# Kernel tuning notes

Measured on AMD Instinct MI355X. Metric: run time of the kernel, lower is better.

The kernel has to match this reference:

```python
import jax, jax.numpy as jnp
import numpy as np

# Static config (matches init_kwargs)
B, H, W, C = 16, 56, 56, 512
WS, SHIFT, NH = 7, 3, 16
HD = C // NH
N = WS * WS
NW = (H // WS) * (W // WS)
SCALE = HD ** -0.5
EPS = 1e-5


def _relative_position_index():
    coords = np.stack(np.meshgrid(np.arange(WS), np.arange(WS), indexing='ij'))  # (2,WS,WS)
    flat = coords.reshape(2, -1)                       # (2,N)
    rel = flat[:, :, None] - flat[:, None, :]          # (2,N,N)
    rel = rel.transpose(1, 2, 0).astype(np.int64)
    rel[..., 0] += WS - 1
    rel[..., 1] += WS - 1
    rel[..., 0] *= 2 * WS - 1
    return rel.sum(-1)                                 # (N,N)


def _window_partition_np(x):
    # x: (H,W) numpy -> (NW, N)
    return x.reshape(H // WS, WS, W // WS, WS).transpose(0, 2, 1, 3).reshape(-1, N)


def _attn_mask():
    img = np.zeros((H, W))
    cnt = 0
    for hs in (slice(0, -WS), slice(-WS, -SHIFT), slice(-SHIFT, None)):
        for ws_ in (slice(0, -WS), slice(-WS, -SHIFT), slice(-SHIFT, None)):
            img[hs, ws_] = cnt
            cnt += 1
    mw = _window_partition_np(img)                     # (NW, N)
    diff = mw[:, None, :] - mw[:, :, None]             # (NW, N, N)
    return np.where(diff != 0, -100.0, 0.0).astype(np.float32)


REL_IDX = jnp.asarray(_relative_position_index())
ATTN_MASK = jnp.asarray(_attn_mask())


def window_partition(x):
    # x: (B,H,W,C) -> (B*NW, N, C)
    x = x.reshape(B, H // WS, WS, W // WS, WS, C)
    return x.transpose(0, 1, 3, 2, 4, 5).reshape(-1, N, C)


def window_reverse(w):
    # w: (B*NW, N, C) -> (B,H,W,C)
    x = w.reshape(B, H // WS, W // WS, WS, WS, C)
    return x.transpose(0, 1, 3, 2, 4, 5).reshape(B, H, W, C)


def layer_norm(x, g, b):
    m = x.mean(-1, keepdims=True)
    v = jnp.mean((x - m) ** 2, axis=-1, keepdims=True)
    return (x - m) * jax.lax.rsqrt(v + EPS) * g + b


def before_cross_attention(x, g, b):
    # x: (B, L, C) -> shifted windows (B*NW, N, C)
    x = layer_norm(x, g, b).reshape(B, H, W, C)
    x = jnp.roll(x, (-SHIFT, -SHIFT), axis=(1, 2))
    return window_partition(x)


def get_qkv(x, Wqkv, bqkv):
    # x: (B_, N, C); Wqkv: (C, 3C)
    qkv = (x @ Wqkv + bqkv).reshape(-1, N, 3, NH, HD).transpose(2, 0, 3, 1, 4)
    return qkv[0], qkv[1], qkv[2]  # each (B_, NH, N, HD)


def setup_inputs() -> dict:
    key = jax.random.key(0)
    ks = jax.random.split(key, 10)
    s = 0.02
    return {
        'rescaled': jax.random.normal(ks[0], (B, H * W, C), jnp.float32),
        'rescaler': jax.random.normal(ks[1], (B, H * W, C), jnp.float32),
        'gamma_a': jnp.ones((C,), jnp.float32),
        'beta_a': jnp.zeros((C,), jnp.float32),
        'gamma_b': jnp.ones((C,), jnp.float32),
        'beta_b': jnp.zeros((C,), jnp.float32),
        'Wqkv_a': jax.random.normal(ks[2], (C, 3 * C), jnp.float32) * s,
        'bqkv_a': jnp.zeros((3 * C,), jnp.float32),
        'Wqkv_b': jax.random.normal(ks[3], (C, 3 * C), jnp.float32) * s,
        'bqkv_b': jnp.zeros((3 * C,), jnp.float32),
        'rpb_table': jax.random.normal(ks[4], ((2 * WS - 1) ** 2, NH), jnp.float32) * s,
        'Wproj': jax.random.normal(ks[5], (C, C), jnp.float32) * s,
        'bproj': jnp.zeros((C,), jnp.float32),
    }


def reference(rescaled, rescaler, gamma_a, beta_a, gamma_b, beta_b,
              Wqkv_a, bqkv_a, Wqkv_b, bqkv_b, rpb_table, Wproj, bproj):
    # norm + shift + window partition for both streams
    xw = before_cross_attention(rescaled, gamma_a, beta_a)   # (B*NW, N, C)
    yw = before_cross_attention(rescaler, gamma_b, beta_b)

    q_a, k_a, v_a = get_qkv(xw, Wqkv_a, bqkv_a)  # rescaled stream
    q_b, k_b, v_b = get_qkv(yw, Wqkv_b, bqkv_b)  # rescaler stream
    # same_key_query=False: q from rescaler, k & v from rescaled
    q, k, v = q_b * SCALE, k_a, v_a

    attn = jnp.einsum('bhnd,bhmd->bhnm', q, k)               # (B*NW, NH, N, N)
    rpb = rpb_table[REL_IDX.reshape(-1)].reshape(N, N, NH).transpose(2, 0, 1)
    attn = attn + rpb[None]
    attn = attn.reshape(B, NW, NH, N, N) + ATTN_MASK[None, :, None]
    attn = jax.nn.softmax(attn.reshape(-1, NH, N, N), axis=-1)

    out = jnp.einsum('bhnm,bhmd->bhnd', attn, v)             # (B*NW, NH, N, HD)
    out = out.transpose(0, 2, 1, 3).reshape(-1, N, C)
    out = out @ Wproj + bproj

    # window reverse + un-shift, back to (B, L, C)
    x = window_reverse(out)
    x = jnp.roll(x, (SHIFT, SHIFT), axis=(1, 2))
    return x.reshape(B, H * W, C)
```

## Files before the change

kernel.cpp:

```cpp
#include <hip/hip_runtime.h>
#include <hip/hip_bf16.h>


typedef short bf16x8 __attribute__((ext_vector_type(8)));
typedef float f32x4 __attribute__((ext_vector_type(4)));
typedef unsigned short u16;

#define MTOT 50176
#define SCALE_ 0.17677669529663687f

__device__ __forceinline__ u16 f2bf(float f) {
    __hip_bfloat16 h = __float2bfloat16(f);
    return *reinterpret_cast<u16*>(&h);
}
__device__ __forceinline__ float bf2f(u16 u) {
    union { unsigned int i; float f; } t; t.i = ((unsigned int)u) << 16; return t.f;
}

#define ASYNC_COPY16(g, l)                                                      \
    __builtin_amdgcn_global_load_lds((__attribute__((address_space(1))) void*)(g), \
                                     (__attribute__((address_space(3))) void*)(l), 16, 0, 0)

__global__ __launch_bounds__(256) void wconv_kernel(
    const float* __restrict__ Wqkv_a, const float* __restrict__ Wqkv_b,
    const float* __restrict__ Wproj, u16* __restrict__ Wt)
{
    const int idx = blockIdx.x * 256 + threadIdx.x;
    const int r = idx >> 9;
    const int k = idx & 511;
    float val;
    if (r < 512)       val = Wqkv_b[k * 1536 + r];
    else if (r < 1536) val = Wqkv_a[k * 1536 + r];
    else               val = Wproj[k * 512 + (r - 1536)];
    Wt[idx] = f2bf(val);
}

__global__ __launch_bounds__(256) void build_bias_kernel(
    const float* __restrict__ rpb, float* __restrict__ biasT)
{
    const int blk = blockIdx.x;
    const int mid = blk >> 4, head = blk & 15;
    const int whq = (mid >> 1) & 1, wwq = mid & 1;
    for (int t = threadIdx.x; t < 4096; t += 256) {
        const int col = t >> 6, row = t & 63;
        float v;
        if (row < 49 && col < 49) {
            const int ih = row / 7, iw = row - ih * 7;
            const int jh = col / 7, jw = col - jh * 7;
            v = rpb[((ih - jh + 6) * 13 + (iw - jw + 6)) * 16 + head];
            const int li = (whq ? (ih < 4 ? 1 : 2) : 0) * 3 + (wwq ? (iw < 4 ? 1 : 2) : 0);
            const int lj = (whq ? (jh < 4 ? 1 : 2) : 0) * 3 + (wwq ? (jw < 4 ? 1 : 2) : 0);
            if (li != lj) v -= 100.0f;
        } else {
            v = -3.0e38f;
        }
        biasT[(size_t)blk * 4096 + t] = v;
    }
}

__device__ __forceinline__ void ln_one(
    const float* __restrict__ src, const float* __restrict__ g,
    const float* __restrict__ bt, u16* __restrict__ dst, int lane)
{
    const float4 v0 = *(const float4*)(src + lane * 8);
    const float4 v1 = *(const float4*)(src + lane * 8 + 4);
    float s = v0.x + v0.y + v0.z + v0.w + v1.x + v1.y + v1.z + v1.w;
    float q = v0.x*v0.x + v0.y*v0.y + v0.z*v0.z + v0.w*v0.w
            + v1.x*v1.x + v1.y*v1.y + v1.z*v1.z + v1.w*v1.w;
#pragma unroll
    for (int o = 32; o >= 1; o >>= 1) { s += __shfl_xor(s, o); q += __shfl_xor(q, o); }
    const float mean = s * (1.0f / 512.0f);
    const float rstd = rsqrtf(q * (1.0f / 512.0f) - mean * mean + 1e-5f);
    const float4 g0 = *(const float4*)(g + lane * 8);
    const float4 g1 = *(const float4*)(g + lane * 8 + 4);
    const float4 b0 = *(const float4*)(bt + lane * 8);
    const float4 b1 = *(const float4*)(bt + lane * 8 + 4);
    u16 o8[8];
    o8[0] = f2bf((v0.x - mean) * rstd * g0.x + b0.x);
    o8[1] = f2bf((v0.y - mean) * rstd * g0.y + b0.y);
    o8[2] = f2bf((v0.z - mean) * rstd * g0.z + b0.z);
    o8[3] = f2bf((v0.w - mean) * rstd * g0.w + b0.w);
    o8[4] = f2bf((v1.x - mean) * rstd * g1.x + b1.x);
    o8[5] = f2bf((v1.y - mean) * rstd * g1.y + b1.y);
    o8[6] = f2bf((v1.z - mean) * rstd * g1.z + b1.z);
    o8[7] = f2bf((v1.w - mean) * rstd * g1.w + b1.w);
    int4 pk;
    pk.x = (int)(((unsigned)o8[1] << 16) | o8[0]);
    pk.y = (int)(((unsigned)o8[3] << 16) | o8[2]);
    pk.z = (int)(((unsigned)o8[5] << 16) | o8[4]);
    pk.w = (int)(((unsigned)o8[7] << 16) | o8[6]);
    *(int4*)(dst + lane * 8) = pk;
}

__global__ __launch_bounds__(256) void ln_window_kernel(
    const float* __restrict__ xa, const float* __restrict__ xb,
    const float* __restrict__ ga, const float* __restrict__ bea,
    const float* __restrict__ gb, const float* __restrict__ beb,
    u16* __restrict__ xw, u16* __restrict__ yw)
{
    const int wave = threadIdx.x >> 6, lane = threadIdx.x & 63;
    const int row = blockIdx.x * 4 + wave;
    const int win = row / 49, n = row - win * 49;
    const int b = win >> 6, wi = win & 63;
    const int wh = wi >> 3, ww = wi & 7;
    const int ih = n / 7, iw = n - ih * 7;
    int h = wh * 7 + ih + 3; if (h >= 56) h -= 56;
    int w = ww * 7 + iw + 3; if (w >= 56) w -= 56;
    const size_t src = ((size_t)b * 3136 + (size_t)h * 56 + w) * 512;
    const size_t dst = (size_t)row * 512;
    ln_one(xa + src, ga, bea, xw + dst, lane);
    ln_one(xb + src, gb, beb, yw + dst, lane);
}

#define GEMM8P_MAIN()                                                           \
    __shared__ __align__(16) u16 As[2][128 * 32];                               \
    __shared__ __align__(16) u16 Bs[2][256 * 32];                               \
    const int tid = threadIdx.x;                                                \
    const int lane = tid & 63;                                                  \
    const int wv = tid >> 6;                                                    \
    const int wm = wv >> 2, wn = wv & 3;                                        \
    const int rowl = lane & 15, kg = lane >> 4;                                 \
    const int fsw = (rowl >> 1) & 3;               \
    f32x4 acc[4][4];                                                            \
    for (int i = 0; i < 4; ++i)                                                 \
        for (int j = 0; j < 4; ++j)                                             \
            acc[i][j] = (f32x4){0.f, 0.f, 0.f, 0.f};                            \
    const int srow = tid >> 2;                                      \
    const int scol = ((tid & 3) ^ ((tid >> 3) & 3)) * 8;      \
    const u16* Ab  = Asrc + (size_t)(mt * 128 + srow) * 512 + scol;             \
    const u16* Bb0 = Bsrc + (size_t)srow * 512 + scol;                          \
    const u16* Bb1 = Bsrc + (size_t)(128 + srow) * 512 + scol;                  \
                                        \
    ASYNC_COPY16(Ab,  (char*)&As[0][0] + tid * 16);                             \
    ASYNC_COPY16(Bb0, (char*)&Bs[0][0] + tid * 16);                             \
    ASYNC_COPY16(Bb1, (char*)&Bs[0][0] + 8192 + tid * 16);                      \
    asm volatile("s_waitcnt vmcnt(0)" ::: "memory");                            \
    __syncthreads();                                                            \
    for (int kt = 0; kt < 16; ++kt) {                                           \
        const int cur = kt & 1, nxt = cur ^ 1;                                  \
        if (kt < 15) {                                                          \
            const int k1 = (kt + 1) * 32;                                       \
            ASYNC_COPY16(Ab + k1,  (char*)&As[0][0] + nxt * 8192 + tid * 16);   \
            ASYNC_COPY16(Bb0 + k1, (char*)&Bs[0][0] + nxt * 16384 + tid * 16);  \
            ASYNC_COPY16(Bb1 + k1, (char*)&Bs[0][0] + nxt * 16384 + 8192 + tid * 16); \
        }                                                                       \
        const u16* Asb = &As[cur][0];                                           \
        const u16* Bsb = &Bs[cur][0];                                           \
        bf16x8 af[4], bfr[4];                                                   \
        _Pragma("unroll")                                                       \
        for (int i = 0; i < 4; ++i)                                             \
            af[i] = *(const bf16x8*)(Asb + (wm * 64 + i * 16 + rowl) * 32       \
                                         + ((kg ^ fsw) * 8));                   \
        _Pragma("unroll")                                                       \
        for (int j = 0; j < 4; ++j)                                             \
            bfr[j] = *(const bf16x8*)(Bsb + (wn * 64 + j * 16 + rowl) * 32      \
                                          + ((kg ^ fsw) * 8));                  \
        _Pragma("unroll")                                                       \
        for (int i = 0; i < 4; ++i) {                                           \
            _Pragma("unroll")                                                   \
            for (int j = 0; j < 4; ++j)                                         \
                acc[i][j] = __builtin_amdgcn_mfma_f32_16x16x32_bf16(            \
                    af[i], bfr[j], acc[i][j], 0, 0, 0);                         \
        }                                                                       \
        asm volatile("s_waitcnt vmcnt(0)" ::: "memory");                        \
        __syncthreads();                                                        \
    }

__global__ __launch_bounds__(512) void gemm_qkv_kernel(
    const u16* __restrict__ xw, const u16* __restrict__ yw,
    const u16* __restrict__ Wt,
    const float* __restrict__ bqkv_a, const float* __restrict__ bqkv_b,
    u16* __restrict__ qb, u16* __restrict__ kb, u16* __restrict__ vb)
{
    const int bid = blockIdx.x;
    const int swz = (bid & 7) * 294 + (bid >> 3);
    const int nt = swz % 6;
    const int mt = swz / 6;
    const u16* Asrc = (nt < 2) ? yw : xw;
    const u16* Bsrc = Wt + (size_t)(nt * 256) * 512;
    GEMM8P_MAIN()

    u16* dst; const float* bvec; bool isq = false;
    if (nt < 2)      { dst = qb; bvec = bqkv_b; isq = true; }
    else if (nt < 4) { dst = kb; bvec = bqkv_a; }
    else             { dst = vb; bvec = bqkv_a; }
#pragma unroll
    for (int j = 0; j < 4; ++j) {
        const int col = nt * 256 + wn * 64 + j * 16 + rowl;
        const float bias_ = bvec[col];
        const int pcol = col & 511;
#pragma unroll
        for (int i = 0; i < 4; ++i) {
#pragma unroll
            for (int rr = 0; rr < 4; ++rr) {
                const int row = mt * 128 + wm * 64 + i * 16 + kg * 4 + rr;
                float val = acc[i][j][rr] + bias_;
                if (isq) val *= SCALE_;
                dst[(size_t)row * 512 + pcol] = f2bf(val);
            }
        }
    }
}

__global__ __launch_bounds__(512) void gemm_proj_kernel(
    const u16* __restrict__ attn_out, const u16* __restrict__ WtProj,
    const float* __restrict__ bproj, float* __restrict__ out)
{
    const int bid = blockIdx.x;
    const int swz = (bid & 7) * 98 + (bid >> 3);
    const int nt = swz & 1;
    const int mt = swz >> 1;
    const u16* Asrc = attn_out;
    const u16* Bsrc = WtProj + (size_t)(nt * 256) * 512;
    GEMM8P_MAIN()

#pragma unroll
    for (int j = 0; j < 4; ++j) {
        const int col = nt * 256 + wn * 64 + j * 16 + rowl;
        const float bias_ = bproj[col];
#pragma unroll
        for (int i = 0; i < 4; ++i) {
#pragma unroll
            for (int rr = 0; rr < 4; ++rr) {
                const int row = mt * 128 + wm * 64 + i * 16 + kg * 4 + rr;
                const int win = row / 49;
                const int nw = row - win * 49;
                const int b = win >> 6, wi = win & 63;
                const int wh = wi >> 3, ww = wi & 7;
                const int ih = nw / 7, iw = nw - ih * 7;
                int h = wh * 7 + ih + 3; if (h >= 56) h -= 56;
                int w = ww * 7 + iw + 3; if (w >= 56) w -= 56;
                out[((size_t)b * 3136 + (size_t)h * 56 + w) * 512 + col] =
                    acc[i][j][rr] + bias_;
            }
        }
    }
}

__global__ __launch_bounds__(256) void attn_kernel(
    const u16* __restrict__ qb, const u16* __restrict__ kb,
    const u16* __restrict__ vb, const float* __restrict__ biasT,
    u16* __restrict__ attn_out)
{
    __shared__ __align__(16) u16 VT[32 * 64];
    __shared__ __align__(16) u16 P[64 * 64];
    const int tid = threadIdx.x;
    const int wh_id = blockIdx.x;
    const int win = wh_id >> 4, head = wh_id & 15;
    const int lane = tid & 63, wvi = tid >> 6;
    const int rowl = lane & 15, kg = lane >> 4;
    const size_t base = (size_t)win * 49 * 512 + head * 32;

    {
        const int j = tid >> 2, d0 = (tid & 3) * 8;
        const bf16x8 v8 = *(const bf16x8*)(vb + base + (size_t)j * 512 + d0);
        const int cj = j >> 3, je = j & 7;
#pragma unroll
        for (int m = 0; m < 8; ++m) {
            const int d = d0 + m;
            VT[d * 64 + ((cj ^ (d & 7)) * 8) + je] = (u16)v8[m];
        }
    }

    const bf16x8 aq = *(const bf16x8*)(qb + base + (size_t)(wvi * 16 + rowl) * 512 + kg * 8);
    f32x4 accS[4];
#pragma unroll
    for (int j = 0; j < 4; ++j) {
        const bf16x8 bk = *(const bf16x8*)(kb + base + (size_t)(j * 16 + rowl) * 512 + kg * 8);
        accS[j] = __builtin_amdgcn_mfma_f32_16x16x32_bf16(
            aq, bk, (f32x4){0.f, 0.f, 0.f, 0.f}, 0, 0, 0);
    }

    const int wi = win & 63;
    const int mid = (((wi >> 3) == 7) ? 2 : 0) + (((wi & 7) == 7) ? 1 : 0);
    const float* bptr = biasT + ((size_t)(mid * 16 + head) << 12);
#pragma unroll
    for (int j = 0; j < 4; ++j) {
        const f32x4 bv4 = *(const f32x4*)(bptr + (j * 16 + rowl) * 64 + wvi * 16 + kg * 4);
#pragma unroll
        for (int r = 0; r < 4; ++r)
            accS[j][r] += bv4[r];
    }

    float rinv[4];
#pragma unroll
    for (int r = 0; r < 4; ++r) {
        float m = fmaxf(fmaxf(accS[0][r], accS[1][r]), fmaxf(accS[2][r], accS[3][r]));
#pragma unroll
        for (int o = 1; o <= 8; o <<= 1) m = fmaxf(m, __shfl_xor(m, o));
        float s = 0.f;
#pragma unroll
        for (int j = 0; j < 4; ++j) {
            accS[j][r] = __expf(accS[j][r] - m);
            s += accS[j][r];
        }
#pragma unroll
        for (int o = 1; o <= 8; o <<= 1) s += __shfl_xor(s, o);
        rinv[r] = __frcp_rn(s);
    }

#pragma unroll
    for (int j = 0; j < 4; ++j) {
        const int c = j * 2 + (rowl >> 3);
#pragma unroll
        for (int r = 0; r < 4; ++r) {
            const int row = wvi * 16 + kg * 4 + r;
            P[row * 64 + ((c ^ (row & 7)) * 8) + (rowl & 7)] = f2bf(accS[j][r]);
        }
    }

    __syncthreads();

    f32x4 accO[2];
#pragma unroll
    for (int dt = 0; dt < 2; ++dt) {
        accO[dt] = (f32x4){0.f, 0.f, 0.f, 0.f};
#pragma unroll
        for (int kb_ = 0; kb_ < 2; ++kb_) {
            const int prow = wvi * 16 + rowl;
            const int ca = kb_ * 4 + kg;
            const bf16x8 ap = *(const bf16x8*)(P + prow * 64 + ((ca ^ (prow & 7)) * 8));
            const int vd = dt * 16 + rowl;
            const bf16x8 bv = *(const bf16x8*)(VT + vd * 64 + ((ca ^ (vd & 7)) * 8));
            accO[dt] = __builtin_amdgcn_mfma_f32_16x16x32_bf16(ap, bv, accO[dt], 0, 0, 0);
        }
    }

#pragma unroll
    for (int dt = 0; dt < 2; ++dt) {
#pragma unroll
        for (int r = 0; r < 4; ++r) {
            const int i = wvi * 16 + kg * 4 + r;
            if (i < 49)
                attn_out[base + (size_t)i * 512 + dt * 16 + rowl] =
                    f2bf(accO[dt][r] * rinv[r]);
        }
    }
}

extern "C" void kernel_launch(void* const* d_in, const int* in_sizes, int n_in,
                              void* d_out, int out_size, void* d_ws, size_t ws_size,
                              hipStream_t stream) {
    (void)in_sizes; (void)n_in; (void)out_size; (void)ws_size;
    const float* rescaled = (const float*)d_in[0];
    const float* rescaler = (const float*)d_in[1];
    const float* gamma_a  = (const float*)d_in[2];
    const float* beta_a   = (const float*)d_in[3];
    const float* gamma_b  = (const float*)d_in[4];
    const float* beta_b   = (const float*)d_in[5];
    const float* Wqkv_a   = (const float*)d_in[6];
    const float* bqkv_a   = (const float*)d_in[7];
    const float* Wqkv_b   = (const float*)d_in[8];
    const float* bqkv_b   = (const float*)d_in[9];
    const float* rpb      = (const float*)d_in[10];
    const float* Wproj    = (const float*)d_in[11];
    const float* bproj    = (const float*)d_in[12];
    float* out = (float*)d_out;

    char* ws = (char*)d_ws;
    const size_t SZ = (size_t)MTOT * 512 * 2;
    u16* xw = (u16*)ws;
    u16* yw = (u16*)(ws + SZ);
    u16* qb = (u16*)(ws + 2 * SZ);
    u16* kb = (u16*)(ws + 3 * SZ);
    u16* vb = (u16*)(ws + 4 * SZ);
    u16* Wt = (u16*)(ws + 5 * SZ);
    float* biasT = (float*)(ws + 5 * SZ + 2097152);
    u16* attn_out = xw;

    wconv_kernel<<<4096, 256, 0, stream>>>(Wqkv_a, Wqkv_b, Wproj, Wt);
    build_bias_kernel<<<64, 256, 0, stream>>>(rpb, biasT);
    ln_window_kernel<<<MTOT / 4, 256, 0, stream>>>(
        rescaled, rescaler, gamma_a, beta_a, gamma_b, beta_b, xw, yw);
    gemm_qkv_kernel<<<2352, 512, 0, stream>>>(
        xw, yw, Wt, bqkv_a, bqkv_b, qb, kb, vb);
    attn_kernel<<<16384, 256, 0, stream>>>(qb, kb, vb, biasT, attn_out);
    gemm_proj_kernel<<<784, 512, 0, stream>>>(
        attn_out, Wt + (size_t)1536 * 512, bproj, out);
}
```

Measured before the change: 534.4 us.

## Overlap GEMM tile loads with MFMA and tile weight transpose through LDS

The shared GEMM main loop now issues the next K-tile's async global-to-LDS copies, waits only for the previous batch with vmcnt(3), and then computes. The last tile is peeled out, so each iteration's loads overlap with its MFMA work instead of being drained with vmcnt(0) after the math. Separately, the weight conversion kernel transposes 64x64 tiles through padded shared memory, using coalesced float4 reads and 16-byte bf16 writes instead of strided scalar reads. This adds an extra barrier per iteration and relies on the vmcnt accounting being correct for the double buffer.

```diff
diff --git a/kernel.cpp b/kernel.cpp
--- a/kernel.cpp
+++ b/kernel.cpp
@@ -25,14 +25,43 @@
     const float* __restrict__ Wqkv_a, const float* __restrict__ Wqkv_b,
     const float* __restrict__ Wproj, u16* __restrict__ Wt)
 {
-    const int idx = blockIdx.x * 256 + threadIdx.x;
-    const int r = idx >> 9;
-    const int k = idx & 511;
-    float val;
-    if (r < 512)       val = Wqkv_b[k * 1536 + r];
-    else if (r < 1536) val = Wqkv_a[k * 1536 + r];
-    else               val = Wproj[k * 512 + (r - 1536)];
-    Wt[idx] = f2bf(val);
+    __shared__ float tile[64][65];
+    const int rt = blockIdx.x >> 3;
+    const int kt = blockIdx.x & 7;
+    const int r0 = rt * 64, k0 = kt * 64;
+    const float* src; int stride, c0;
+    if (r0 < 512)       { src = Wqkv_b; stride = 1536; c0 = r0; }
+    else if (r0 < 1536) { src = Wqkv_a; stride = 1536; c0 = r0; }
+    else                { src = Wproj;  stride = 512;  c0 = r0 - 1536; }
+
+    const int tid = threadIdx.x;
+    const int sr = tid >> 4, sc = (tid & 15) * 4;
+#pragma unroll
+    for (int p = 0; p < 4; ++p) {
+        const int k = sr + p * 16;
+        const float4 v = *(const float4*)(src + (size_t)(k0 + k) * stride + c0 + sc);
+        tile[k][sc] = v.x; tile[k][sc + 1] = v.y;
+        tile[k][sc + 2] = v.z; tile[k][sc + 3] = v.w;
+    }
+    __syncthreads();
+
+    const int dc = tid >> 2;
+    const int kk = (tid & 3) * 16;
+    u16 o[16];
+#pragma unroll
+    for (int m = 0; m < 16; ++m) o[m] = f2bf(tile[kk + m][dc]);
+    int4 pk0, pk1;
+    pk0.x = (int)(((unsigned)o[1] << 16) | o[0]);
+    pk0.y = (int)(((unsigned)o[3] << 16) | o[2]);
+    pk0.z = (int)(((unsigned)o[5] << 16) | o[4]);
+    pk0.w = (int)(((unsigned)o[7] << 16) | o[6]);
+    pk1.x = (int)(((unsigned)o[9] << 16) | o[8]);
+    pk1.y = (int)(((unsigned)o[11] << 16) | o[10]);
+    pk1.z = (int)(((unsigned)o[13] << 16) | o[12]);
+    pk1.w = (int)(((unsigned)o[15] << 16) | o[14]);
+    u16* dst = Wt + (size_t)(r0 + dc) * 512 + k0 + kk;
+    *(int4*)dst = pk0;
+    *(int4*)(dst + 8) = pk1;
 }
 
 __global__ __launch_bounds__(256) void build_bias_kernel(
@@ -130,20 +159,18 @@
     const u16* Ab  = Asrc + (size_t)(mt * 128 + srow) * 512 + scol;             \
     const u16* Bb0 = Bsrc + (size_t)srow * 512 + scol;                          \
     const u16* Bb1 = Bsrc + (size_t)(128 + srow) * 512 + scol;                  \
-                                        \
+                       \
     ASYNC_COPY16(Ab,  (char*)&As[0][0] + tid * 16);                             \
     ASYNC_COPY16(Bb0, (char*)&Bs[0][0] + tid * 16);                             \
     ASYNC_COPY16(Bb1, (char*)&Bs[0][0] + 8192 + tid * 16);                      \
-    asm volatile("s_waitcnt vmcnt(0)" ::: "memory");                            \
-    __syncthreads();                                                            \
-    for (int kt = 0; kt < 16; ++kt) {                                           \
+    for (int kt = 0; kt < 15; ++kt) {                                           \
         const int cur = kt & 1, nxt = cur ^ 1;                                  \
-        if (kt < 15) {                                                          \
-            const int k1 = (kt + 1) * 32;                                       \
-            ASYNC_COPY16(Ab + k1,  (char*)&As[0][0] + nxt * 8192 + tid * 16);   \
-            ASYNC_COPY16(Bb0 + k1, (char*)&Bs[0][0] + nxt * 16384 + tid * 16);  \
-            ASYNC_COPY16(Bb1 + k1, (char*)&Bs[0][0] + nxt * 16384 + 8192 + tid * 16); \
-        }                                                                       \
+        const int k1 = (kt + 1) * 32;                                           \
+        ASYNC_COPY16(Ab + k1,  (char*)&As[0][0] + nxt * 8192 + tid * 16);       \
+        ASYNC_COPY16(Bb0 + k1, (char*)&Bs[0][0] + nxt * 16384 + tid * 16);      \
+        ASYNC_COPY16(Bb1 + k1, (char*)&Bs[0][0] + nxt * 16384 + 8192 + tid * 16); \
+        asm volatile("s_waitcnt vmcnt(3)" ::: "memory");                        \
+        __syncthreads();                                                        \
         const u16* Asb = &As[cur][0];                                           \
         const u16* Bsb = &Bs[cur][0];                                           \
         bf16x8 af[4], bfr[4];                                                   \
@@ -162,8 +189,30 @@
                 acc[i][j] = __builtin_amdgcn_mfma_f32_16x16x32_bf16(            \
                     af[i], bfr[j], acc[i][j], 0, 0, 0);                         \
         }                                                                       \
-        asm volatile("s_waitcnt vmcnt(0)" ::: "memory");                        \
         __syncthreads();                                                        \
+    }                                                                           \
+                               \
+    asm volatile("s_waitcnt vmcnt(0)" ::: "memory");                            \
+    __syncthreads();                                                            \
+    {                                                                           \
+        const u16* Asb = &As[1][0];                                             \
+        const u16* Bsb = &Bs[1][0];                                             \
+        bf16x8 af[4], bfr[4];                                                   \
+        _Pragma("unroll")                                                       \
+        for (int i = 0; i < 4; ++i)                                             \
+            af[i] = *(const bf16x8*)(Asb + (wm * 64 + i * 16 + rowl) * 32       \
+                                         + ((kg ^ fsw) * 8));                   \
+        _Pragma("unroll")                                                       \
+        for (int j = 0; j < 4; ++j)                                             \
+            bfr[j] = *(const bf16x8*)(Bsb + (wn * 64 + j * 16 + rowl) * 32      \
+                                          + ((kg ^ fsw) * 8));                  \
+        _Pragma("unroll")                                                       \
+        for (int i = 0; i < 4; ++i) {                                           \
+            _Pragma("unroll")                                                   \
+            for (int j = 0; j < 4; ++j)                                         \
+                acc[i][j] = __builtin_amdgcn_mfma_f32_16x16x32_bf16(            \
+                    af[i], bfr[j], acc[i][j], 0, 0, 0);                         \
+        }                                                                       \
     }
 
 __global__ __launch_bounds__(512) void gemm_qkv_kernel(
@@ -368,7 +417,7 @@
     float* biasT = (float*)(ws + 5 * SZ + 2097152);
     u16* attn_out = xw;
 
-    wconv_kernel<<<4096, 256, 0, stream>>>(Wqkv_a, Wqkv_b, Wproj, Wt);
+    wconv_kernel<<<256, 256, 0, stream>>>(Wqkv_a, Wqkv_b, Wproj, Wt);
     build_bias_kernel<<<64, 256, 0, stream>>>(rpb, biasT);
     ln_window_kernel<<<MTOT / 4, 256, 0, stream>>>(
         rescaled, rescaler, gamma_a, beta_a, gamma_b, beta_b, xw, yw);
```

Measured after the change: 557.2 us. 1.04x slower.
